# Kernel optimization log

Measured on AMD Instinct MI355X. Metric: run time of the kernel, lower is better.

## Reference

```python
import jax, jax.numpy as jnp
import numpy as np

HIDDEN = 1024
HEADS = 16
HEAD_DIM = HIDDEN // HEADS  # 64
ROPE_BASE = 10000.0
CLAMP = 10000.0


def _rope_cos_sin(seq_len, dtype=jnp.float32):
    inv_freq = 1.0 / (ROPE_BASE ** (jnp.arange(0, HEAD_DIM, 2, dtype=dtype) / HEAD_DIM))
    t = jnp.arange(seq_len, dtype=dtype)
    freqs = jnp.outer(t, inv_freq)  # [T, HEAD_DIM//2]
    return jnp.cos(freqs), jnp.sin(freqs)


def _apply_rope(x, cos, sin):
    # x: [B, H, T, HEAD_DIM]; cos/sin: [T, HEAD_DIM//2]
    x1, x2 = jnp.split(x, 2, axis=-1)
    cos = cos[None, None]
    sin = sin[None, None]
    return jnp.concatenate([x1 * cos - x2 * sin, x1 * sin + x2 * cos], axis=-1)


def setup_inputs() -> dict:
    key = jax.random.key(0)
    ks = jax.random.split(key, 5)
    B, T, D = 2, 2048, HIDDEN
    x = jax.random.normal(ks[0], (B, T, D), dtype=jnp.float32)
    # torch Linear weights are [out, in]; init std=0.02, zero bias
    Wq = jax.random.normal(ks[1], (D, D), dtype=jnp.float32) * 0.02
    Wk = jax.random.normal(ks[2], (D, D), dtype=jnp.float32) * 0.02
    Wv = jax.random.normal(ks[3], (D, D), dtype=jnp.float32) * 0.02
    Wo = jax.random.normal(ks[4], (D, D), dtype=jnp.float32) * 0.02
    bq = jnp.zeros((D,), jnp.float32)
    bk = jnp.zeros((D,), jnp.float32)
    bv = jnp.zeros((D,), jnp.float32)
    bo = jnp.zeros((D,), jnp.float32)
    # causal mask: True where attention is disallowed (strict upper triangle)
    causal_mask = jnp.triu(jnp.ones((T, T), dtype=bool), k=1)[None, None]
    return {"x": x, "causal_mask": causal_mask,
            "Wq": Wq, "bq": bq, "Wk": Wk, "bk": bk,
            "Wv": Wv, "bv": bv, "Wo": Wo, "bo": bo}


def reference(x, causal_mask, Wq, bq, Wk, bk, Wv, bv, Wo, bo):
    B, T, D = x.shape
    H, hd = HEADS, HEAD_DIM

    def proj(W, b):
        y = jnp.einsum('btd,ed->bte', x, W) + b
        return y.reshape(B, T, H, hd).transpose(0, 2, 1, 3)  # [B,H,T,hd]

    q = proj(Wq, bq)
    k = proj(Wk, bk)
    v = proj(Wv, bv)

    cos, sin = _rope_cos_sin(T, x.dtype)
    q = _apply_rope(q, cos, sin)
    k = _apply_rope(k, cos, sin)

    scores = jnp.einsum('bhqd,bhkd->bhqk', q, k) / jnp.sqrt(jnp.asarray(hd, x.dtype))
    # masked_fill(-inf) happens BEFORE clamp, so masked entries become -10000
    scores = jnp.where(causal_mask[:, :, :T, :T], -jnp.inf, scores)
    scores = jnp.clip(scores, -CLAMP, CLAMP)
    attn = jax.nn.softmax(scores, axis=-1)
    out = jnp.einsum('bhqk,bhkd->bhqd', attn, v)
    out = out.transpose(0, 2, 1, 3).reshape(B, T, D)
    return jnp.einsum('btd,ed->bte', out, Wo) + bo
```

## Files before the change

kernel.cpp:

```cpp
#include <hip/hip_runtime.h>
#include <hip/hip_bf16.h>
#include <math.h>

#define T_SEQ   2048
#define D_MOD   1024
#define N_HEADS 16
#define HEAD_DIM 64
#define B_BATCH 2
#define M_ROWS  (B_BATCH * T_SEQ)

typedef unsigned short u16;
typedef unsigned int u32;
typedef __attribute__((ext_vector_type(8))) short short8;
typedef __attribute__((ext_vector_type(4))) float floatx4;
typedef __attribute__((ext_vector_type(16))) float f32x16;
typedef __attribute__((ext_vector_type(4))) u32 u32x4;

__device__ inline floatx4 mfma16(short8 a, short8 b, floatx4 c) {
  return __builtin_amdgcn_mfma_f32_16x16x32_bf16(a, b, c, 0, 0, 0);
}
__device__ inline f32x16 mfma32(short8 a, short8 b, f32x16 c) {
  return __builtin_amdgcn_mfma_f32_32x32x16_bf16(a, b, c, 0, 0, 0);
}

__device__ inline u16 f2bf(float f) {
  __hip_bfloat16 h = __float2bfloat16(f);
  return __builtin_bit_cast(u16, h);
}
__device__ inline u32 pack2bf(float lo, float hi) {
  return (u32)f2bf(lo) | ((u32)f2bf(hi) << 16);
}

__device__ inline void gload16(const void* g, void* s) {
  __builtin_amdgcn_global_load_lds(
      (const __attribute__((address_space(1))) void*)g,
      (__attribute__((address_space(3))) void*)s, 16, 0, 0);
}

__global__ void cast_all_kernel(const float* __restrict__ x,
                                const float* __restrict__ Wq, const float* __restrict__ Wk,
                                const float* __restrict__ Wv, const float* __restrict__ Wo,
                                u16* __restrict__ Xb, u16* __restrict__ Wqb, u16* __restrict__ Wkb,
                                u16* __restrict__ Wvb, u16* __restrict__ Wob) {
  size_t i4 = ((size_t)blockIdx.x * 256 + threadIdx.x) * 4;
  size_t seg = i4 >> 20;
  const float* src; u16* dst; size_t off;
  if (seg < 4)       { src = x;  dst = Xb;  off = i4; }
  else if (seg == 4) { src = Wq; dst = Wqb; off = i4 - ((size_t)4 << 20); }
  else if (seg == 5) { src = Wk; dst = Wkb; off = i4 - ((size_t)5 << 20); }
  else if (seg == 6) { src = Wv; dst = Wvb; off = i4 - ((size_t)6 << 20); }
  else               { src = Wo; dst = Wob; off = i4 - ((size_t)7 << 20); }
  float4 v = *(const float4*)(src + off);
  ushort4 o;
  o.x = f2bf(v.x); o.y = f2bf(v.y); o.z = f2bf(v.z); o.w = f2bf(v.w);
  *(ushort4*)(dst + off) = o;
}

__global__ void rope_table_kernel(float* __restrict__ cosT, float* __restrict__ sinT) {
  int tid = blockIdx.x * blockDim.x + threadIdx.x;
  int t = tid >> 5, j = tid & 31;
  double inv = pow(10000.0, -((double)(2 * j) / 64.0));
  double a = (double)t * inv;
  cosT[tid] = (float)cos(a);
  sinT[tid] = (float)sin(a);
}

template<int OUT_BF16, int DO_ROPE>
__global__ __launch_bounds__(256) void gemm128_kernel(
    const u16* __restrict__ A,
    const u16* __restrict__ W0, const u16* __restrict__ W1, const u16* __restrict__ W2,
    const float* __restrict__ b0, const float* __restrict__ b1, const float* __restrict__ b2,
    void* __restrict__ C0, void* __restrict__ C1, void* __restrict__ C2,
    const float* __restrict__ cosT, const float* __restrict__ sinT) {
  const int z = blockIdx.z;
  const u16*  W    = (z == 0) ? W0 : (z == 1 ? W1 : W2);
  const float* bias = (z == 0) ? b0 : (z == 1 ? b1 : b2);
  void*       C    = (z == 0) ? C0 : (z == 1 ? C1 : C2);
  const int K = D_MOD, N = D_MOD;

  __shared__ __align__(16) char smem[34816];
  u16* lA0 = (u16*)smem;
  u16* lA1 = (u16*)(smem + 8192);
  u16* lB0 = (u16*)(smem + 16384);
  u16* lB1 = (u16*)(smem + 24576);

  const int tid = threadIdx.x;
  const int w = tid >> 6, l = tid & 63, g = l >> 4, ln = l & 15;
  const int wr = w >> 1, wc = w & 1;
  const int m0 = blockIdx.y * 128, n0 = blockIdx.x * 128;

  floatx4 acc[4][4];
#pragma unroll
  for (int mi = 0; mi < 4; ++mi)
#pragma unroll
    for (int ni = 0; ni < 4; ++ni) acc[mi][ni] = (floatx4){0.f, 0.f, 0.f, 0.f};

  auto stage = [&](u16* la, u16* lb, int kk) {
#pragma unroll
    for (int p = 0; p < 2; ++p) {
      int c = p * 256 + w * 64 + l;
      int r = c >> 2, cc = c & 3;
      gload16(A + (size_t)(m0 + r) * K + kk + cc * 8, la + (p * 256 + w * 64) * 8);
      gload16(W + (size_t)(n0 + r) * K + kk + cc * 8, lb + (p * 256 + w * 64) * 8);
    }
  };

  stage(lA0, lB0, 0);
  __syncthreads();
  for (int t = 0; t < K / 32; ++t) {
    u16* la = (t & 1) ? lA1 : lA0;
    u16* lb = (t & 1) ? lB1 : lB0;
    if (t + 1 < K / 32) stage((t & 1) ? lA0 : lA1, (t & 1) ? lB0 : lB1, (t + 1) * 32);
    short8 af[4], bf[4];
#pragma unroll
    for (int mi = 0; mi < 4; ++mi)
      af[mi] = *(const short8*)&la[(wr * 64 + mi * 16 + ln) * 32 + g * 8];
#pragma unroll
    for (int ni = 0; ni < 4; ++ni)
      bf[ni] = *(const short8*)&lb[(wc * 64 + ni * 16 + ln) * 32 + g * 8];
#pragma unroll
    for (int mi = 0; mi < 4; ++mi)
#pragma unroll
      for (int ni = 0; ni < 4; ++ni)
        acc[mi][ni] = mfma16(af[mi], bf[ni], acc[mi][ni]);
    __syncthreads();
  }

  float bv[4];
#pragma unroll
  for (int ni = 0; ni < 4; ++ni) bv[ni] = bias[n0 + wc * 64 + ni * 16 + ln];

  if (DO_ROPE && z == 2) {
    u16* pt = (u16*)smem;
#pragma unroll
    for (int mi = 0; mi < 4; ++mi)
#pragma unroll
      for (int ni = 0; ni < 4; ++ni)
#pragma unroll
        for (int r = 0; r < 4; ++r)
          pt[(wc * 64 + ni * 16 + ln) * 136 + wr * 64 + mi * 16 + g * 4 + r] =
              f2bf(acc[mi][ni][r] + bv[ni]);
    __syncthreads();
    u16* Vt = (u16*)C;
    const int b = m0 >> 11, tc0 = m0 & (T_SEQ - 1);
#pragma unroll
    for (int i = 0; i < 8; ++i) {
      const int c = tid + 256 * i;
      const int row = c >> 4, mc = c & 15;
      const int n = n0 + row;
      const int hh = n >> 6, d = n & 63;
      short8 val = *(const short8*)&pt[row * 136 + mc * 8];
      *(short8*)(Vt + ((size_t)(b * N_HEADS + hh) * 64 + d) * T_SEQ + tc0 + mc * 8) = val;
    }
    return;
  }

#pragma unroll
  for (int mi = 0; mi < 4; ++mi) {
#pragma unroll
    for (int r = 0; r < 4; ++r) {
      const int m = m0 + wr * 64 + mi * 16 + g * 4 + r;
      if (DO_ROPE && z < 2) {
        const int t = m & (T_SEQ - 1);
#pragma unroll
        for (int ni = 0; ni < 2; ++ni) {
          const int j = ni * 16 + ln;
          float cv = cosT[t * 32 + j], sv = sinT[t * 32 + j];
          float v1 = acc[mi][ni][r] + bv[ni];
          float v2 = acc[mi][ni + 2][r] + bv[ni + 2];
          ((u16*)C)[(size_t)m * N + n0 + wc * 64 + j]      = f2bf(v1 * cv - v2 * sv);
          ((u16*)C)[(size_t)m * N + n0 + wc * 64 + j + 32] = f2bf(v1 * sv + v2 * cv);
        }
      } else {
#pragma unroll
        for (int ni = 0; ni < 4; ++ni) {
          float v = acc[mi][ni][r] + bv[ni];
          size_t idx = (size_t)m * N + n0 + wc * 64 + ni * 16 + ln;
          if (OUT_BF16) ((u16*)C)[idx] = f2bf(v);
          else          ((float*)C)[idx] = v;
        }
      }
    }
  }
}

__global__ __launch_bounds__(256) void flash5_kernel(const u16* __restrict__ Q, const u16* __restrict__ Kb,
                                                     const u16* __restrict__ Vt, u16* __restrict__ O) {
  const int tid = threadIdx.x;
  const int w = tid >> 6, l = tid & 63;
  const int lq = l & 31, hi = l >> 5;

  const int orig = blockIdx.x;
  const int wg = (orig & 7) * 64 + (orig >> 3);
  const int bh = wg >> 4;
  const int qg = wg & 15;
  const int qt = (w == 0) ? qg : (w == 1) ? 63 - qg : (w == 2) ? 31 - qg : 32 + qg;
  const int q0 = qt * 32;
  const int b = bh >> 4, h = bh & 15;

  const u16* Qh = Q  + (size_t)b * T_SEQ * D_MOD + h * HEAD_DIM;
  const u16* Kh = Kb + (size_t)b * T_SEQ * D_MOD + h * HEAD_DIM;
  const u16* Vh = Vt + (size_t)bh * 64 * T_SEQ;

  short8 qf[4];
  {
    const u16* qp = Qh + (size_t)(q0 + lq) * D_MOD + 8 * hi;
#pragma unroll
    for (int j = 0; j < 4; ++j) qf[j] = *(const short8*)(qp + 16 * j);
  }

  f32x16 o0, o1;
#pragma unroll
  for (int r = 0; r < 16; ++r) { o0[r] = 0.f; o1[r] = 0.f; }
  float m_r = -INFINITY, l_r = 0.f;

  const int ntiles = (qt >> 1) + 1;
  for (int kt = 0; kt < ntiles; ++kt) {
    const int k0 = kt * 64;
    const bool last = (kt == ntiles - 1);

    short8 kf0[4], kf1[4], vf0[4], vf1[4];
    {
      const u16* kp0 = Kh + (size_t)(k0 + lq) * D_MOD + 8 * hi;
      const u16* kp1 = kp0 + 32 * D_MOD;
#pragma unroll
      for (int j = 0; j < 4; ++j) {
        kf0[j] = *(const short8*)(kp0 + 16 * j);
        kf1[j] = *(const short8*)(kp1 + 16 * j);
      }
      const u16* vp0 = Vh + (size_t)lq * T_SEQ + k0 + 8 * hi;
      const u16* vp1 = vp0 + 32 * T_SEQ;
#pragma unroll
      for (int js = 0; js < 4; ++js) {
        vf0[js] = *(const short8*)(vp0 + 16 * js);
        vf1[js] = *(const short8*)(vp1 + 16 * js);
      }
    }

    f32x16 s0, s1;
#pragma unroll
    for (int r = 0; r < 16; ++r) { s0[r] = 0.f; s1[r] = 0.f; }
    __builtin_amdgcn_s_setprio(1);
#pragma unroll
    for (int j = 0; j < 4; ++j) {
      s0 = mfma32(kf0[j], qf[j], s0);
      s1 = mfma32(kf1[j], qf[j], s1);
    }
    __builtin_amdgcn_s_setprio(0);

    float p[32];
#pragma unroll
    for (int r = 0; r < 16; ++r) { p[r] = s0[r] * 0.125f; p[16 + r] = s1[r] * 0.125f; }
    if (last) {
      const int qrow = q0 + lq;
#pragma unroll
      for (int r = 0; r < 16; ++r) {
        const int kv = k0 + (r & 3) + 8 * (r >> 2) + 4 * hi;
        if (kv > qrow) p[r] = -10000.0f;
        if (kv + 32 > qrow) p[16 + r] = -10000.0f;
      }
    }

    float mx = p[0];
#pragma unroll
    for (int i = 1; i < 32; ++i) mx = fmaxf(mx, p[i]);
    mx = fmaxf(mx, __shfl_xor(mx, 32));

    const float mnew = fmaxf(m_r, mx);
    const float alpha = __expf(m_r - mnew);
    l_r *= alpha;
#pragma unroll
    for (int r = 0; r < 16; ++r) { o0[r] *= alpha; o1[r] *= alpha; }
    m_r = mnew;
#pragma unroll
    for (int i = 0; i < 32; ++i) p[i] = __expf(p[i] - m_r);
    float sum = 0.f;
#pragma unroll
    for (int i = 0; i < 32; ++i) sum += p[i];
    sum += __shfl_xor(sum, 32);
    l_r += sum;

    u32x4 fw[4];
#pragma unroll
    for (int a = 0; a < 2; ++a) {
      u32 W[8];
#pragma unroll
      for (int j = 0; j < 8; ++j) W[j] = pack2bf(p[16 * a + 2 * j], p[16 * a + 2 * j + 1]);
      u32 A0 = __shfl_xor(hi ? W[0] : W[2], 32);
      u32 A1 = __shfl_xor(hi ? W[1] : W[3], 32);
      u32 B0 = __shfl_xor(hi ? W[4] : W[6], 32);
      u32 B1 = __shfl_xor(hi ? W[5] : W[7], 32);
      fw[2 * a]     = (u32x4){hi ? A0 : W[0], hi ? A1 : W[1], hi ? W[2] : A0, hi ? W[3] : A1};
      fw[2 * a + 1] = (u32x4){hi ? B0 : W[4], hi ? B1 : W[5], hi ? W[6] : B0, hi ? W[7] : B1};
    }

    __builtin_amdgcn_s_setprio(1);
#pragma unroll
    for (int js = 0; js < 4; ++js) {
      short8 pf = __builtin_bit_cast(short8, fw[js]);
      o0 = mfma32(vf0[js], pf, o0);
      o1 = mfma32(vf1[js], pf, o1);
    }
    __builtin_amdgcn_s_setprio(0);
  }

  const float inv = 1.0f / l_r;
  u16* op = O + (size_t)b * T_SEQ * D_MOD + (size_t)(q0 + lq) * D_MOD + h * HEAD_DIM;
#pragma unroll
  for (int a = 0; a < 2; ++a) {
#pragma unroll
    for (int rq = 0; rq < 4; ++rq) {
      const int d0 = 32 * a + 8 * rq + 4 * hi;
      ushort4 st;
      st.x = f2bf(((a == 0) ? o0[4 * rq + 0] : o1[4 * rq + 0]) * inv);
      st.y = f2bf(((a == 0) ? o0[4 * rq + 1] : o1[4 * rq + 1]) * inv);
      st.z = f2bf(((a == 0) ? o0[4 * rq + 2] : o1[4 * rq + 2]) * inv);
      st.w = f2bf(((a == 0) ? o0[4 * rq + 3] : o1[4 * rq + 3]) * inv);
      *(ushort4*)(op + d0) = st;
    }
  }
}

extern "C" void kernel_launch(void* const* d_in, const int* in_sizes, int n_in,
                              void* d_out, int out_size, void* d_ws, size_t ws_size,
                              hipStream_t stream) {
  const float* x  = (const float*)d_in[0];
  const float* Wq = (const float*)d_in[2];
  const float* bq = (const float*)d_in[3];
  const float* Wk = (const float*)d_in[4];
  const float* bk = (const float*)d_in[5];
  const float* Wv = (const float*)d_in[6];
  const float* bv = (const float*)d_in[7];
  const float* Wo = (const float*)d_in[8];
  const float* bo = (const float*)d_in[9];
  float* out = (float*)d_out;

  char* ws = (char*)d_ws;
  const size_t MB = 1024 * 1024;
  u16* Xb   = (u16*)(ws + 0);
  u16* Ab   = (u16*)(ws + 0);
  u16* Wqb  = (u16*)(ws + 8 * MB);
  u16* Wkb  = (u16*)(ws + 10 * MB);
  u16* Wvb  = (u16*)(ws + 12 * MB);
  u16* Wob  = (u16*)(ws + 14 * MB);
  u16* Qb   = (u16*)(ws + 16 * MB);
  u16* Kb   = (u16*)(ws + 24 * MB);
  u16* Vt   = (u16*)(ws + 32 * MB);
  float* cosT = (float*)(ws + 48 * MB);
  float* sinT = (float*)(ws + 48 * MB + 256 * 1024);

  cast_all_kernel<<<8192, 256, 0, stream>>>(x, Wq, Wk, Wv, Wo, Xb, Wqb, Wkb, Wvb, Wob);
  rope_table_kernel<<<256, 256, 0, stream>>>(cosT, sinT);

  gemm128_kernel<1, 1><<<dim3(8, 32, 3), 256, 0, stream>>>(
      Xb, Wqb, Wkb, Wvb, bq, bk, bv, Qb, Kb, Vt, cosT, sinT);

  flash5_kernel<<<dim3(512), 256, 0, stream>>>(Qb, Kb, Vt, Ab);

  gemm128_kernel<0, 0><<<dim3(8, 32, 1), 256, 0, stream>>>(
      Ab, Wob, Wob, Wob, bo, bo, bo, out, out, out, nullptr, nullptr);
}
```

Measured before the change: 235.5 us.

## Double-buffer K prefetch, skip masked half of diagonal tile, remap query tiles

The flash attention loop now prefetches the next key tile into alternating register buffers while the current tile is computed, so global loads overlap with MFMA and softmax work. The final diagonal tile is specialised: for even query tiles only the first 32 keys are computed, which skips fully masked MFMAs and exp work. The query-tile assignment changes so the four waves in a block take consecutive tiles instead of the earlier balanced pairing, giving each block similar but unequal per-wave loop counts. The extra K buffers raise register pressure, and the new mapping may leave waves within a block idle at different times.

```diff
diff --git a/kernel.cpp b/kernel.cpp
--- a/kernel.cpp
+++ b/kernel.cpp
@@ -184,7 +184,7 @@
   }
 }
 
-__global__ __launch_bounds__(256) void flash5_kernel(const u16* __restrict__ Q, const u16* __restrict__ Kb,
+__global__ __launch_bounds__(256) void flash6_kernel(const u16* __restrict__ Q, const u16* __restrict__ Kb,
                                                      const u16* __restrict__ Vt, u16* __restrict__ O) {
   const int tid = threadIdx.x;
   const int w = tid >> 6, l = tid & 63;
@@ -194,7 +194,7 @@
   const int wg = (orig & 7) * 64 + (orig >> 3);
   const int bh = wg >> 4;
   const int qg = wg & 15;
-  const int qt = (w == 0) ? qg : (w == 1) ? 63 - qg : (w == 2) ? 31 - qg : 32 + qg;
+  const int qt = (15 - qg) * 4 + w;
   const int q0 = qt * 32;
   const int b = bh >> 4, h = bh & 15;
 
@@ -214,95 +214,167 @@
   for (int r = 0; r < 16; ++r) { o0[r] = 0.f; o1[r] = 0.f; }
   float m_r = -INFINITY, l_r = 0.f;
 
+  short8 kf0A[4], kf1A[4], kf0B[4], kf1B[4], vf0[4], vf1[4];
+
+#define PREF_K(KF0, KF1, K0) { \
+  const u16* kp0_ = Kh + (size_t)((K0) + lq) * D_MOD + 8 * hi; \
+  const u16* kp1_ = kp0_ + 32 * D_MOD; \
+  _Pragma("unroll") for (int j_ = 0; j_ < 4; ++j_) { \
+    KF0[j_] = *(const short8*)(kp0_ + 16 * j_); \
+    KF1[j_] = *(const short8*)(kp1_ + 16 * j_); } }
+
+#define PREF_V(K0) { \
+  const u16* vp0_ = Vh + (size_t)lq * T_SEQ + (K0) + 8 * hi; \
+  const u16* vp1_ = vp0_ + 32 * T_SEQ; \
+  _Pragma("unroll") for (int j_ = 0; j_ < 4; ++j_) { \
+    vf0[j_] = *(const short8*)(vp0_ + 16 * j_); \
+    vf1[j_] = *(const short8*)(vp1_ + 16 * j_); } }
+
+#define TILE_FULL(KF0, KF1) { \
+  f32x16 s0_, s1_; \
+  _Pragma("unroll") for (int r_ = 0; r_ < 16; ++r_) { s0_[r_] = 0.f; s1_[r_] = 0.f; } \
+  __builtin_amdgcn_s_setprio(1); \
+  _Pragma("unroll") for (int j_ = 0; j_ < 4; ++j_) { \
+    s0_ = mfma32(KF0[j_], qf[j_], s0_); \
+    s1_ = mfma32(KF1[j_], qf[j_], s1_); } \
+  __builtin_amdgcn_s_setprio(0); \
+  float p_[32]; \
+  _Pragma("unroll") for (int r_ = 0; r_ < 16; ++r_) { \
+    p_[r_] = s0_[r_] * 0.125f; p_[16 + r_] = s1_[r_] * 0.125f; } \
+  float mx_ = p_[0]; \
+  _Pragma("unroll") for (int i_ = 1; i_ < 32; ++i_) mx_ = fmaxf(mx_, p_[i_]); \
+  mx_ = fmaxf(mx_, __shfl_xor(mx_, 32)); \
+  const float mnew_ = fmaxf(m_r, mx_); \
+  const float alpha_ = __expf(m_r - mnew_); \
+  l_r *= alpha_; \
+  _Pragma("unroll") for (int r_ = 0; r_ < 16; ++r_) { o0[r_] *= alpha_; o1[r_] *= alpha_; } \
+  m_r = mnew_; \
+  _Pragma("unroll") for (int i_ = 0; i_ < 32; ++i_) p_[i_] = __expf(p_[i_] - m_r); \
+  float sum_ = 0.f; \
+  _Pragma("unroll") for (int i_ = 0; i_ < 32; ++i_) sum_ += p_[i_]; \
+  sum_ += __shfl_xor(sum_, 32); \
+  l_r += sum_; \
+  u32x4 fw_[4]; \
+  _Pragma("unroll") for (int a_ = 0; a_ < 2; ++a_) { \
+    u32 W_[8]; \
+    _Pragma("unroll") for (int j_ = 0; j_ < 8; ++j_) \
+      W_[j_] = pack2bf(p_[16 * a_ + 2 * j_], p_[16 * a_ + 2 * j_ + 1]); \
+    u32 A0_ = __shfl_xor(hi ? W_[0] : W_[2], 32); \
+    u32 A1_ = __shfl_xor(hi ? W_[1] : W_[3], 32); \
+    u32 B0_ = __shfl_xor(hi ? W_[4] : W_[6], 32); \
+    u32 B1_ = __shfl_xor(hi ? W_[5] : W_[7], 32); \
+    fw_[2 * a_]     = (u32x4){hi ? A0_ : W_[0], hi ? A1_ : W_[1], hi ? W_[2] : A0_, hi ? W_[3] : A1_}; \
+    fw_[2 * a_ + 1] = (u32x4){hi ? B0_ : W_[4], hi ? B1_ : W_[5], hi ? W_[6] : B0_, hi ? W_[7] : B1_}; } \
+  __builtin_amdgcn_s_setprio(1); \
+  _Pragma("unroll") for (int j_ = 0; j_ < 4; ++j_) { \
+    short8 pf_ = __builtin_bit_cast(short8, fw_[j_]); \
+    o0 = mfma32(vf0[j_], pf_, o0); \
+    o1 = mfma32(vf1[j_], pf_, o1); } \
+  __builtin_amdgcn_s_setprio(0); }
+
+#define TILE_LAST(KF0, KF1, K0L) { \
+  const int qrow_ = q0 + lq; \
+  f32x16 s0_; \
+  _Pragma("unroll") for (int r_ = 0; r_ < 16; ++r_) s0_[r_] = 0.f; \
+  __builtin_amdgcn_s_setprio(1); \
+  _Pragma("unroll") for (int j_ = 0; j_ < 4; ++j_) s0_ = mfma32(KF0[j_], qf[j_], s0_); \
+  __builtin_amdgcn_s_setprio(0); \
+  if ((qt & 1) == 0) { \
+    float p_[16]; \
+    _Pragma("unroll") for (int r_ = 0; r_ < 16; ++r_) { \
+      const int kv_ = (K0L) + (r_ & 3) + 8 * (r_ >> 2) + 4 * hi; \
+      p_[r_] = (kv_ > qrow_) ? -10000.0f : s0_[r_] * 0.125f; } \
+    float mx_ = p_[0]; \
+    _Pragma("unroll") for (int i_ = 1; i_ < 16; ++i_) mx_ = fmaxf(mx_, p_[i_]); \
+    mx_ = fmaxf(mx_, __shfl_xor(mx_, 32)); \
+    const float mnew_ = fmaxf(m_r, mx_); \
+    const float alpha_ = __expf(m_r - mnew_); \
+    l_r *= alpha_; \
+    _Pragma("unroll") for (int r_ = 0; r_ < 16; ++r_) { o0[r_] *= alpha_; o1[r_] *= alpha_; } \
+    m_r = mnew_; \
+    _Pragma("unroll") for (int i_ = 0; i_ < 16; ++i_) p_[i_] = __expf(p_[i_] - m_r); \
+    float sum_ = 0.f; \
+    _Pragma("unroll") for (int i_ = 0; i_ < 16; ++i_) sum_ += p_[i_]; \
+    sum_ += __shfl_xor(sum_, 32); \
+    l_r += sum_; \
+    u32x4 fw_[2]; \
+    { u32 W_[8]; \
+      _Pragma("unroll") for (int j_ = 0; j_ < 8; ++j_) W_[j_] = pack2bf(p_[2 * j_], p_[2 * j_ + 1]); \
+      u32 A0_ = __shfl_xor(hi ? W_[0] : W_[2], 32); \
+      u32 A1_ = __shfl_xor(hi ? W_[1] : W_[3], 32); \
+      u32 B0_ = __shfl_xor(hi ? W_[4] : W_[6], 32); \
+      u32 B1_ = __shfl_xor(hi ? W_[5] : W_[7], 32); \
+      fw_[0] = (u32x4){hi ? A0_ : W_[0], hi ? A1_ : W_[1], hi ? W_[2] : A0_, hi ? W_[3] : A1_}; \
+      fw_[1] = (u32x4){hi ? B0_ : W_[4], hi ? B1_ : W_[5], hi ? W_[6] : B0_, hi ? W_[7] : B1_}; } \
+    __builtin_amdgcn_s_setprio(1); \
+    _Pragma("unroll") for (int j_ = 0; j_ < 2; ++j_) { \
+      short8 pf_ = __builtin_bit_cast(short8, fw_[j_]); \
+      o0 = mfma32(vf0[j_], pf_, o0); \
+      o1 = mfma32(vf1[j_], pf_, o1); } \
+    __builtin_amdgcn_s_setprio(0); \
+  } else { \
+    f32x16 s1_; \
+    _Pragma("unroll") for (int r_ = 0; r_ < 16; ++r_) s1_[r_] = 0.f; \
+    __builtin_amdgcn_s_setprio(1); \
+    _Pragma("unroll") for (int j_ = 0; j_ < 4; ++j_) s1_ = mfma32(KF1[j_], qf[j_], s1_); \
+    __builtin_amdgcn_s_setprio(0); \
+    float p_[32]; \
+    _Pragma("unroll") for (int r_ = 0; r_ < 16; ++r_) { \
+      p_[r_] = s0_[r_] * 0.125f; \
+      const int kv_ = (K0L) + 32 + (r_ & 3) + 8 * (r_ >> 2) + 4 * hi; \
+      p_[16 + r_] = (kv_ > qrow_) ? -10000.0f : s1_[r_] * 0.125f; } \
+    float mx_ = p_[0]; \
+    _Pragma("unroll") for (int i_ = 1; i_ < 32; ++i_) mx_ = fmaxf(mx_, p_[i_]); \
+    mx_ = fmaxf(mx_, __shfl_xor(mx_, 32)); \
+    const float mnew_ = fmaxf(m_r, mx_); \
+    const float alpha_ = __expf(m_r - mnew_); \
+    l_r *= alpha_; \
+    _Pragma("unroll") for (int r_ = 0; r_ < 16; ++r_) { o0[r_] *= alpha_; o1[r_] *= alpha_; } \
+    m_r = mnew_; \
+    _Pragma("unroll") for (int i_ = 0; i_ < 32; ++i_) p_[i_] = __expf(p_[i_] - m_r); \
+    float sum_ = 0.f; \
+    _Pragma("unroll") for (int i_ = 0; i_ < 32; ++i_) sum_ += p_[i_]; \
+    sum_ += __shfl_xor(sum_, 32); \
+    l_r += sum_; \
+    u32x4 fw_[4]; \
+    _Pragma("unroll") for (int a_ = 0; a_ < 2; ++a_) { \
+      u32 W_[8]; \
+      _Pragma("unroll") for (int j_ = 0; j_ < 8; ++j_) \
+        W_[j_] = pack2bf(p_[16 * a_ + 2 * j_], p_[16 * a_ + 2 * j_ + 1]); \
+      u32 A0_ = __shfl_xor(hi ? W_[0] : W_[2], 32); \
+      u32 A1_ = __shfl_xor(hi ? W_[1] : W_[3], 32); \
+      u32 B0_ = __shfl_xor(hi ? W_[4] : W_[6], 32); \
+      u32 B1_ = __shfl_xor(hi ? W_[5] : W_[7], 32); \
+      fw_[2 * a_]     = (u32x4){hi ? A0_ : W_[0], hi ? A1_ : W_[1], hi ? W_[2] : A0_, hi ? W_[3] : A1_}; \
+      fw_[2 * a_ + 1] = (u32x4){hi ? B0_ : W_[4], hi ? B1_ : W_[5], hi ? W_[6] : B0_, hi ? W_[7] : B1_}; } \
+    __builtin_amdgcn_s_setprio(1); \
+    _Pragma("unroll") for (int j_ = 0; j_ < 4; ++j_) { \
+      short8 pf_ = __builtin_bit_cast(short8, fw_[j_]); \
+      o0 = mfma32(vf0[j_], pf_, o0); \
+      o1 = mfma32(vf1[j_], pf_, o1); } \
+    __builtin_amdgcn_s_setprio(0); } }
+
   const int ntiles = (qt >> 1) + 1;
-  for (int kt = 0; kt < ntiles; ++kt) {
-    const int k0 = kt * 64;
-    const bool last = (kt == ntiles - 1);
-
-    short8 kf0[4], kf1[4], vf0[4], vf1[4];
-    {
-      const u16* kp0 = Kh + (size_t)(k0 + lq) * D_MOD + 8 * hi;
-      const u16* kp1 = kp0 + 32 * D_MOD;
-#pragma unroll
-      for (int j = 0; j < 4; ++j) {
-        kf0[j] = *(const short8*)(kp0 + 16 * j);
-        kf1[j] = *(const short8*)(kp1 + 16 * j);
-      }
-      const u16* vp0 = Vh + (size_t)lq * T_SEQ + k0 + 8 * hi;
-      const u16* vp1 = vp0 + 32 * T_SEQ;
-#pragma unroll
-      for (int js = 0; js < 4; ++js) {
-        vf0[js] = *(const short8*)(vp0 + 16 * js);
-        vf1[js] = *(const short8*)(vp1 + 16 * js);
-      }
+  PREF_K(kf0A, kf1A, 0);
+  int t = 0;
+  while (t + 1 < ntiles) {
+    PREF_V(t * 64);
+    PREF_K(kf0B, kf1B, (t + 1) * 64);
+    TILE_FULL(kf0A, kf1A);
+    ++t;
+    if (t + 1 >= ntiles) {
+      PREF_V(t * 64);
+      TILE_LAST(kf0B, kf1B, t * 64);
+      goto flash_done;
     }
-
-    f32x16 s0, s1;
-#pragma unroll
-    for (int r = 0; r < 16; ++r) { s0[r] = 0.f; s1[r] = 0.f; }
-    __builtin_amdgcn_s_setprio(1);
-#pragma unroll
-    for (int j = 0; j < 4; ++j) {
-      s0 = mfma32(kf0[j], qf[j], s0);
-      s1 = mfma32(kf1[j], qf[j], s1);
-    }
-    __builtin_amdgcn_s_setprio(0);
-
-    float p[32];
-#pragma unroll
-    for (int r = 0; r < 16; ++r) { p[r] = s0[r] * 0.125f; p[16 + r] = s1[r] * 0.125f; }
-    if (last) {
-      const int qrow = q0 + lq;
-#pragma unroll
-      for (int r = 0; r < 16; ++r) {
-        const int kv = k0 + (r & 3) + 8 * (r >> 2) + 4 * hi;
-        if (kv > qrow) p[r] = -10000.0f;
-        if (kv + 32 > qrow) p[16 + r] = -10000.0f;
-      }
-    }
-
-    float mx = p[0];
-#pragma unroll
-    for (int i = 1; i < 32; ++i) mx = fmaxf(mx, p[i]);
-    mx = fmaxf(mx, __shfl_xor(mx, 32));
-
-    const float mnew = fmaxf(m_r, mx);
-    const float alpha = __expf(m_r - mnew);
-    l_r *= alpha;
-#pragma unroll
-    for (int r = 0; r < 16; ++r) { o0[r] *= alpha; o1[r] *= alpha; }
-    m_r = mnew;
-#pragma unroll
-    for (int i = 0; i < 32; ++i) p[i] = __expf(p[i] - m_r);
-    float sum = 0.f;
-#pragma unroll
-    for (int i = 0; i < 32; ++i) sum += p[i];
-    sum += __shfl_xor(sum, 32);
-    l_r += sum;
-
-    u32x4 fw[4];
-#pragma unroll
-    for (int a = 0; a < 2; ++a) {
-      u32 W[8];
-#pragma unroll
-      for (int j = 0; j < 8; ++j) W[j] = pack2bf(p[16 * a + 2 * j], p[16 * a + 2 * j + 1]);
-      u32 A0 = __shfl_xor(hi ? W[0] : W[2], 32);
-      u32 A1 = __shfl_xor(hi ? W[1] : W[3], 32);
-      u32 B0 = __shfl_xor(hi ? W[4] : W[6], 32);
-      u32 B1 = __shfl_xor(hi ? W[5] : W[7], 32);
-      fw[2 * a]     = (u32x4){hi ? A0 : W[0], hi ? A1 : W[1], hi ? W[2] : A0, hi ? W[3] : A1};
-      fw[2 * a + 1] = (u32x4){hi ? B0 : W[4], hi ? B1 : W[5], hi ? W[6] : B0, hi ? W[7] : B1};
-    }
-
-    __builtin_amdgcn_s_setprio(1);
-#pragma unroll
-    for (int js = 0; js < 4; ++js) {
-      short8 pf = __builtin_bit_cast(short8, fw[js]);
-      o0 = mfma32(vf0[js], pf, o0);
-      o1 = mfma32(vf1[js], pf, o1);
-    }
-    __builtin_amdgcn_s_setprio(0);
-  }
+    PREF_V(t * 64);
+    PREF_K(kf0A, kf1A, (t + 1) * 64);
+    TILE_FULL(kf0B, kf1B);
+    ++t;
+  }
+  PREF_V(t * 64);
+  TILE_LAST(kf0A, kf1A, t * 64);
+flash_done:;
 
   const float inv = 1.0f / l_r;
   u16* op = O + (size_t)b * T_SEQ * D_MOD + (size_t)(q0 + lq) * D_MOD + h * HEAD_DIM;
@@ -355,7 +427,7 @@
   gemm128_kernel<1, 1><<<dim3(8, 32, 3), 256, 0, stream>>>(
       Xb, Wqb, Wkb, Wvb, bq, bk, bv, Qb, Kb, Vt, cosT, sinT);
 
-  flash5_kernel<<<dim3(512), 256, 0, stream>>>(Qb, Kb, Vt, Ab);
+  flash6_kernel<<<dim3(512), 256, 0, stream>>>(Qb, Kb, Vt, Ab);
 
   gemm128_kernel<0, 0><<<dim3(8, 32, 1), 256, 0, stream>>>(
       Ab, Wob, Wob, Wob, bo, bo, bo, out, out, out, nullptr, nullptr);
```

Result: slower. 262.6 us (+11.5%).

## Split KV loop across four waves per query tile with LDS merge

Applied to the files above, without the earlier changes.

Each workgroup now handles a single 32-row query tile, and its four waves split the key tiles round-robin rather than each wave owning a different query tile. The partial softmax states (max, sum, output accumulators) of waves 1-3 are written to shared memory, and wave 0 rescales and merges them before writing. The grid grows from 512 to 2048 blocks to expose more parallelism and shorten the critical path for long causal rows. In exchange it adds LDS traffic, a block barrier and a serial merge on one wave, and leaves idle waves on short rows.

```diff
diff --git a/kernel.cpp b/kernel.cpp
--- a/kernel.cpp
+++ b/kernel.cpp
@@ -184,17 +184,19 @@
   }
 }
 
-__global__ __launch_bounds__(256) void flash5_kernel(const u16* __restrict__ Q, const u16* __restrict__ Kb,
+__global__ __launch_bounds__(256) void flash7_kernel(const u16* __restrict__ Q, const u16* __restrict__ Kb,
                                                      const u16* __restrict__ Vt, u16* __restrict__ O) {
+  __shared__ float og[3][32][64];
+  __shared__ float mlg[3][2][64];
+
   const int tid = threadIdx.x;
   const int w = tid >> 6, l = tid & 63;
   const int lq = l & 31, hi = l >> 5;
 
   const int orig = blockIdx.x;
-  const int wg = (orig & 7) * 64 + (orig >> 3);
-  const int bh = wg >> 4;
-  const int qg = wg & 15;
-  const int qt = (w == 0) ? qg : (w == 1) ? 63 - qg : (w == 2) ? 31 - qg : 32 + qg;
+  const int wg = (orig & 7) * 256 + (orig >> 3);
+  const int bh = wg >> 6;
+  const int qt = 63 - (wg & 63);
   const int q0 = qt * 32;
   const int b = bh >> 4, h = bh & 15;
 
@@ -215,7 +217,7 @@
   float m_r = -INFINITY, l_r = 0.f;
 
   const int ntiles = (qt >> 1) + 1;
-  for (int kt = 0; kt < ntiles; ++kt) {
+  for (int kt = w; kt < ntiles; kt += 4) {
     const int k0 = kt * 64;
     const bool last = (kt == ntiles - 1);
 
@@ -304,7 +306,37 @@
     __builtin_amdgcn_s_setprio(0);
   }
 
-  const float inv = 1.0f / l_r;
+  if (w > 0) {
+    mlg[w - 1][0][l] = m_r;
+    mlg[w - 1][1][l] = l_r;
+#pragma unroll
+    for (int r = 0; r < 16; ++r) {
+      og[w - 1][r][l]      = o0[r];
+      og[w - 1][16 + r][l] = o1[r];
+    }
+  }
+  __syncthreads();
+  if (w != 0) return;
+
+  float m = m_r;
+#pragma unroll
+  for (int pi = 0; pi < 3; ++pi) m = fmaxf(m, mlg[pi][0][l]);
+  const float aS = __expf(m_r - m);
+  float lsum = l_r * aS;
+#pragma unroll
+  for (int r = 0; r < 16; ++r) { o0[r] *= aS; o1[r] *= aS; }
+#pragma unroll
+  for (int pi = 0; pi < 3; ++pi) {
+    const float ap = __expf(mlg[pi][0][l] - m);
+    lsum += mlg[pi][1][l] * ap;
+#pragma unroll
+    for (int r = 0; r < 16; ++r) {
+      o0[r] += og[pi][r][l] * ap;
+      o1[r] += og[pi][16 + r][l] * ap;
+    }
+  }
+
+  const float inv = 1.0f / lsum;
   u16* op = O + (size_t)b * T_SEQ * D_MOD + (size_t)(q0 + lq) * D_MOD + h * HEAD_DIM;
 #pragma unroll
   for (int a = 0; a < 2; ++a) {
@@ -355,7 +387,7 @@
   gemm128_kernel<1, 1><<<dim3(8, 32, 3), 256, 0, stream>>>(
       Xb, Wqb, Wkb, Wvb, bq, bk, bv, Qb, Kb, Vt, cosT, sinT);
 
-  flash5_kernel<<<dim3(512), 256, 0, stream>>>(Qb, Kb, Vt, Ab);
+  flash7_kernel<<<dim3(2048), 256, 0, stream>>>(Qb, Kb, Vt, Ab);
 
   gemm128_kernel<0, 0><<<dim3(8, 32, 1), 256, 0, stream>>>(
       Ab, Wob, Wob, Wob, bo, bo, bo, out, out, out, nullptr, nullptr);
```

Measured after the change: 238.3 us. About the same (+1.2%).
